# Kernel tuning notes

Measured on AMD Instinct MI355X. Metric: run time of the kernel, lower is better.

Reference implementation:

```python
import jax, jax.numpy as jnp
import numpy as np

N = 10000
IN_DIM = 256
HID = 256
HEADS = 8
NUM_CLASSES = 40
EPS = 1e-5
NEG_SLOPE = 0.2


def gat_conv(x, src, dst, W, a_src, a_dst, bias, concat):
    # x: [N, F_in]; W: [F_in, H*C]; a_src/a_dst: [H, C]
    n = x.shape[0]
    H, C = a_src.shape
    h = (x @ W).reshape(n, H, C)                       # [N,H,C]
    s_src = jnp.einsum('nhc,hc->nh', h, a_src)         # [N,H]
    s_dst = jnp.einsum('nhc,hc->nh', h, a_dst)         # [N,H]
    score = jax.nn.leaky_relu(s_src[src] + s_dst[dst], NEG_SLOPE)  # [E,H]
    m = jax.lax.stop_gradient(jax.ops.segment_max(score, dst, num_segments=n))
    e = jnp.exp(score - m[dst])                        # [E,H]
    denom = jax.ops.segment_sum(e, dst, num_segments=n)
    alpha = e / denom[dst]                             # per-dst edge softmax
    msg = h[src] * alpha[:, :, None]                   # [E,H,C]
    out = jax.ops.segment_sum(msg, dst, num_segments=n)  # [N,H,C]
    out = out.reshape(n, H * C) if concat else out.mean(axis=1)
    return out + bias


def batch_norm(x, gamma, beta):
    mu = x.mean(axis=0)
    var = x.var(axis=0)
    return gamma * (x - mu) * jax.lax.rsqrt(var + EPS) + beta


def setup_inputs() -> dict:
    key = jax.random.key(0)
    ks = jax.random.split(key, 16)
    C0 = HID // HEADS  # 32, concat layer
    x = jax.random.normal(ks[0], (N, IN_DIM), jnp.float32)
    edge_index = jax.random.randint(ks[1], (2, 160000), 0, N, jnp.int32)
    def lin(k, fi, fo):
        return jax.random.normal(k, (fi, fo), jnp.float32) / np.sqrt(fi)
    return {
        'x': x,
        'edge_index': edge_index,
        'W0': lin(ks[2], IN_DIM, HEADS * C0),
        'a_src0': jax.random.normal(ks[3], (HEADS, C0), jnp.float32) * 0.1,
        'a_dst0': jax.random.normal(ks[4], (HEADS, C0), jnp.float32) * 0.1,
        'b0': jnp.zeros((HID,), jnp.float32),
        'g0': jnp.ones((HID,), jnp.float32),
        'be0': jnp.zeros((HID,), jnp.float32),
        'W1': lin(ks[5], HID, HEADS * HID),
        'a_src1': jax.random.normal(ks[6], (HEADS, HID), jnp.float32) * 0.1,
        'a_dst1': jax.random.normal(ks[7], (HEADS, HID), jnp.float32) * 0.1,
        'b1': jnp.zeros((HID,), jnp.float32),
        'g1': jnp.ones((HID,), jnp.float32),
        'be1': jnp.zeros((HID,), jnp.float32),
        'Wc': lin(ks[8], HID, NUM_CLASSES),
        'bc': jnp.zeros((NUM_CLASSES,), jnp.float32),
    }


def reference(x, edge_index, W0, a_src0, a_dst0, b0, g0, be0,
              W1, a_src1, a_dst1, b1, g1, be1, Wc, bc):
    n = x.shape[0]
    loops = jnp.arange(n, dtype=edge_index.dtype)
    src = jnp.concatenate([edge_index[0], loops])  # add_self_loops=True
    dst = jnp.concatenate([edge_index[1], loops])

    # layer 0: concat=True -> [N, 256]
    h = gat_conv(x, src, dst, W0, a_src0, a_dst0, b0, concat=True)
    h = jax.nn.elu(batch_norm(h, g0, be0))
    # i==0: no residual; dropout is identity at eval

    # layer 1 (last): concat=False (mean over heads) -> [N, 256]
    h_in = h
    h = gat_conv(h, src, dst, W1, a_src1, a_dst1, b1, concat=False)
    h = jax.nn.elu(batch_norm(h, g1, be1)) + h_in  # residual for i>0

    return h @ Wc + bc  # logits [N, num_classes]
```

## Files before the change

### kernel.cpp

```cpp
#include <hip/hip_runtime.h>
#include <math.h>

#define NN 10000
#define HEADS 8
#define NCLS 40
#define CHK 64
#define LOG2E 1.4426950408889634f

typedef __attribute__((ext_vector_type(8))) short short8;
typedef __attribute__((ext_vector_type(4))) float floatx4;

static __device__ __forceinline__ short f2bf(float f) {
    unsigned u = __builtin_bit_cast(unsigned, f);
    unsigned r = (u + 0x7fff + ((u >> 16) & 1)) >> 16;
    return (short)r;
}
static __device__ __forceinline__ float bf2f(unsigned short u) {
    unsigned x = ((unsigned)u) << 16;
    return __builtin_bit_cast(float, x);
}
static __device__ __forceinline__ void gl2lds16(const void* g, void* l) {
    __builtin_amdgcn_global_load_lds(
        (const __attribute__((address_space(1))) unsigned int*)g,
        (__attribute__((address_space(3))) unsigned int*)l, 16, 0, 0);
}

__global__ __launch_bounds__(256) void gemm_bf16_v3(
    const short* __restrict__ A, const short* __restrict__ Bt,
    float* __restrict__ C, short* __restrict__ Cbf, const float* __restrict__ bias,
    float* __restrict__ stats, int M, int Nn, int K, float alpha)
{
    __shared__ short As[64 * 64];
    __shared__ short Bs[64 * 64];
    const int tid = threadIdx.x;
    const int w = tid >> 6, L = tid & 63;
    const int quad = L >> 4, lr = L & 15;
    const int col0 = blockIdx.x * 64, row0 = blockIdx.y * 64;

    const int srow = w * 16 + (L >> 3);
    const int schunk = (L & 7) ^ (L >> 3);
    int ga0 = row0 + srow;     if (ga0 > M - 1)  ga0 = M - 1;
    int ga1 = row0 + srow + 8; if (ga1 > M - 1)  ga1 = M - 1;
    int gb0 = col0 + srow;     if (gb0 > Nn - 1) gb0 = Nn - 1;
    int gb1 = col0 + srow + 8; if (gb1 > Nn - 1) gb1 = Nn - 1;
    const short* agp0 = A + (size_t)ga0 * K + schunk * 8;
    const short* agp1 = A + (size_t)ga1 * K + schunk * 8;
    const short* bgp0 = Bt + (size_t)gb0 * K + schunk * 8;
    const short* bgp1 = Bt + (size_t)gb1 * K + schunk * 8;
    short* alp0 = &As[w * 1024];
    short* alp1 = &As[w * 1024 + 512];
    short* blp0 = &Bs[w * 1024];
    short* blp1 = &Bs[w * 1024 + 512];

    floatx4 acc[4];
    const floatx4 zf = {0.f, 0.f, 0.f, 0.f};
    #pragma unroll
    for (int i = 0; i < 4; i++) acc[i] = zf;

    for (int k0 = 0; k0 < K; k0 += 64) {
        gl2lds16(agp0 + k0, alp0);
        gl2lds16(agp1 + k0, alp1);
        gl2lds16(bgp0 + k0, blp0);
        gl2lds16(bgp1 + k0, blp1);
        __syncthreads();
        #pragma unroll
        for (int ks = 0; ks < 2; ks++) {
            const int sl = ((ks * 4 + quad) ^ (lr & 7)) * 8;
            short8 bfr = *(const short8*)&Bs[(w * 16 + lr) * 64 + sl];
            #pragma unroll
            for (int i = 0; i < 4; i++) {
                short8 afr = *(const short8*)&As[(i * 16 + lr) * 64 + sl];
                acc[i] = __builtin_amdgcn_mfma_f32_16x16x32_bf16(afr, bfr, acc[i], 0, 0, 0);
            }
        }
        __syncthreads();
    }
    const int ccol = col0 + w * 16 + lr;
    float s = 0.f, s2 = 0.f;
    if (ccol < Nn) {
        float bv = bias ? bias[ccol] : 0.f;
        #pragma unroll
        for (int i = 0; i < 4; i++) {
            #pragma unroll
            for (int r = 0; r < 4; r++) {
                int crow = row0 + i * 16 + quad * 4 + r;
                if (crow < M) {
                    float v = alpha * acc[i][r] + bv;
                    if (C)   C[(size_t)crow * Nn + ccol] = v;
                    if (Cbf) Cbf[(size_t)crow * Nn + ccol] = f2bf(v);
                    s += v; s2 += v * v;
                }
            }
        }
    }
    if (stats) {
        s  += __shfl_xor(s, 16, 64);  s  += __shfl_xor(s, 32, 64);
        s2 += __shfl_xor(s2, 16, 64); s2 += __shfl_xor(s2, 32, 64);
        if (L < 16 && ccol < Nn) {
            atomicAdd(&stats[ccol], s);
            atomicAdd(&stats[256 + ccol], s2);
        }
    }
}

__global__ void count_edges_kernel(const int* __restrict__ dst, int* counts, int E) {
    int e = blockIdx.x * 256 + threadIdx.x;
    if (e < E) atomicAdd(&counts[dst[e]], 1);
}

__global__ __launch_bounds__(1024) void scan_kernel(
    int* counts, int* offsets, int* cursor, int* elist, int n)
{
    const int P = (n + 1023) >> 10;
    __shared__ int wsum[16];
    int tid = threadIdx.x, lane = tid & 63, wid = tid >> 6;
    int base = tid * P;
    int local[16];
    int deg[16];
    int s = 0;
    for (int j = 0; j < P; j++) {
        int i = base + j;
        local[j] = s;
        deg[j] = (i < n) ? counts[i] + 1 : 0;
        s += deg[j];
    }
    int inc = s;
    #pragma unroll
    for (int off = 1; off < 64; off <<= 1) {
        int tv = __shfl_up(inc, off, 64);
        if (lane >= off) inc += tv;
    }
    if (lane == 63) wsum[wid] = inc;
    __syncthreads();
    if (tid < 16) {
        int v = wsum[tid];
        int winc = v;
        #pragma unroll
        for (int off = 1; off < 16; off <<= 1) {
            int tv = __shfl_up(winc, off, 16);
            if (tid >= off) winc += tv;
        }
        wsum[tid] = winc - v;
    }
    __syncthreads();
    int excl = inc - s + wsum[wid];
    for (int j = 0; j < P; j++) {
        int i = base + j;
        if (i < n) {
            int o = excl + local[j];
            counts[i] = deg[j];
            offsets[i] = o;
            elist[o] = i;
            cursor[i] = o + 1;
        }
    }
}

__global__ void scatter_edges_kernel(const int* __restrict__ src, const int* __restrict__ dst,
                                     int* cursor, int* elist, int E) {
    int e = blockIdx.x * 256 + threadIdx.x;
    if (e < E) {
        int d = dst[e];
        int pos = atomicAdd(&cursor[d], 1);
        elist[pos] = src[e];
    }
}

__global__ __launch_bounds__(256) void prep_all(
    const float* __restrict__ x, const float* __restrict__ W0,
    const float* __restrict__ W1, const float* __restrict__ a_src1,
    const float* __restrict__ a_dst1, const float* __restrict__ Wc,
    short* __restrict__ xb, short* __restrict__ W0T, float* __restrict__ v1,
    short* __restrict__ W1pT, short* __restrict__ WcT)
{
    __shared__ float tile[32][33];
    const int b = blockIdx.x, t = threadIdx.x;
    if (b < 2500) {
        int i = b * 256 + t;
        floatx4 v = ((const floatx4*)x)[i];
        short4 o = {f2bf(v[0]), f2bf(v[1]), f2bf(v[2]), f2bf(v[3])};
        ((short4*)xb)[i] = o;
    } else if (b < 2756) {
        int o = b - 2500;
        W0T[o * 256 + t] = f2bf(W0[t * 256 + o]);
    } else if (b < 2772) {
        int idx = (b - 2756) * 256 + t;
        int f = idx >> 4, j = idx & 15;
        int h = j & 7;
        const float* a = (j < 8) ? a_src1 : a_dst1;
        float s = 0.f;
        for (int c = 0; c < 256; c++)
            s += W1[f * 2048 + h * 256 + c] * a[h * 256 + c];
        v1[idx] = s;
    } else if (b < 3284) {
        int id = b - 2772;
        int h = id >> 6, f0 = ((id >> 3) & 7) * 32, c0 = (id & 7) * 32;
        int tx = t & 31, ty = t >> 5;
        for (int r = ty; r < 32; r += 8)
            tile[r][tx] = W1[(size_t)(f0 + r) * 2048 + h * 256 + c0 + tx];
        __syncthreads();
        for (int r = ty; r < 32; r += 8)
            W1pT[(size_t)(c0 + r) * 2048 + h * 256 + f0 + tx] = f2bf(tile[tx][r]);
    } else {
        int o = b - 3284;
        WcT[o * 256 + t] = f2bf(Wc[t * 40 + o]);
    }
}

__global__ __launch_bounds__(256) void score0_wave(
    const unsigned short* __restrict__ h0b, const float* __restrict__ a_src,
    const float* __restrict__ a_dst, float* __restrict__ s0)
{
    const int wid = threadIdx.x >> 6, L = threadIdx.x & 63;
    const int n = blockIdx.x * 4 + wid;
    if (n >= NN) return;
    ushort4 vv = *(const ushort4*)(h0b + (size_t)n * 256 + 4 * L);
    floatx4 as = *(const floatx4*)(a_src + 4 * L);
    floatx4 ad = *(const floatx4*)(a_dst + 4 * L);
    float v0 = bf2f(vv.x), v1_ = bf2f(vv.y), v2 = bf2f(vv.z), v3 = bf2f(vv.w);
    float ps = v0 * as[0] + v1_ * as[1] + v2 * as[2] + v3 * as[3];
    float pd = v0 * ad[0] + v1_ * ad[1] + v2 * ad[2] + v3 * ad[3];
    #pragma unroll
    for (int off = 1; off < 8; off <<= 1) {
        ps += __shfl_xor(ps, off, 64);
        pd += __shfl_xor(pd, off, 64);
    }
    if ((L & 7) == 0) {
        s0[n * 16 + (L >> 3)] = ps;
        s0[n * 16 + 8 + (L >> 3)] = pd;
    }
}

__global__ __launch_bounds__(256) void agg0_fused(
    const unsigned short* __restrict__ h0b, const float* __restrict__ s0,
    const int* __restrict__ offsets, const int* __restrict__ counts,
    const int* __restrict__ elist, float* __restrict__ out)
{
    __shared__ float pw_s[4][CHK * 8];
    __shared__ int   sn_s[4][CHK];
    const int wid = threadIdx.x >> 6, L = threadIdx.x & 63;
    const int n = blockIdx.x * 4 + wid;
    if (n >= NN) return;
    float* pw = pw_s[wid];
    int*   sw = sn_s[wid];
    const int deg = counts[n], start = offsets[n];
    const int hL = L >> 3;

    floatx4 sda = *(const floatx4*)(s0 + n * 16 + 8);
    floatx4 sdb = *(const floatx4*)(s0 + n * 16 + 12);
    float sd[8] = {sda[0], sda[1], sda[2], sda[3], sdb[0], sdb[1], sdb[2], sdb[3]};
    float lp[8] = {0.f, 0.f, 0.f, 0.f, 0.f, 0.f, 0.f, 0.f};
    float a0 = 0.f, a1 = 0.f, a2 = 0.f, a3 = 0.f;

    for (int e0 = 0; e0 < deg; e0 += CHK) {
        int ch = deg - e0; if (ch > CHK) ch = CHK;
        if (L < ch) {
            int sn = elist[start + e0 + L];
            sw[L] = sn;
            floatx4 ssa = *(const floatx4*)(s0 + sn * 16);
            floatx4 ssb = *(const floatx4*)(s0 + sn * 16 + 4);
            float ss[8] = {ssa[0], ssa[1], ssa[2], ssa[3], ssb[0], ssb[1], ssb[2], ssb[3]};
            float p[8];
            #pragma unroll
            for (int h = 0; h < 8; h++) {
                float v = ss[h] + sd[h];
                v = (v > 0.f) ? v : 0.2f * v;
                p[h] = exp2f(v * LOG2E);
                lp[h] += p[h];
            }
            floatx4 p0 = {p[0], p[1], p[2], p[3]};
            floatx4 p1 = {p[4], p[5], p[6], p[7]};
            *(floatx4*)&pw[L * 8] = p0;
            *(floatx4*)&pw[L * 8 + 4] = p1;
        }
        for (int e = 0; e < ch; e++) {
            float wgt = pw[e * 8 + hL];
            ushort4 vv = *(const ushort4*)(h0b + (size_t)sw[e] * 256 + 4 * L);
            a0 += wgt * bf2f(vv.x);
            a1 += wgt * bf2f(vv.y);
            a2 += wgt * bf2f(vv.z);
            a3 += wgt * bf2f(vv.w);
        }
    }
    #pragma unroll
    for (int off = 1; off < 64; off <<= 1)
        #pragma unroll
        for (int h = 0; h < 8; h++)
            lp[h] += __shfl_xor(lp[h], off, 64);
    float inv = 1.f / lp[hL];
    floatx4 o = {a0 * inv, a1 * inv, a2 * inv, a3 * inv};
    *(floatx4*)(out + (size_t)n * 256 + 4 * L) = o;
}

__global__ __launch_bounds__(256) void agg1_fused(
    const unsigned short* __restrict__ hb, const float* __restrict__ s1,
    const int* __restrict__ offsets, const int* __restrict__ counts,
    const int* __restrict__ elist, short* __restrict__ aggout)
{
    __shared__ float pw_s[4][CHK * 8];
    __shared__ int   sn_s[4][CHK];
    const int wid = threadIdx.x >> 6, L = threadIdx.x & 63;
    const int n = blockIdx.x * 4 + wid;
    if (n >= NN) return;
    float* pw = pw_s[wid];
    int*   sw = sn_s[wid];
    const int deg = counts[n], start = offsets[n];

    floatx4 sda = *(const floatx4*)(s1 + n * 16 + 8);
    floatx4 sdb = *(const floatx4*)(s1 + n * 16 + 12);
    float sd[8] = {sda[0], sda[1], sda[2], sda[3], sdb[0], sdb[1], sdb[2], sdb[3]};
    float lp[8] = {0.f, 0.f, 0.f, 0.f, 0.f, 0.f, 0.f, 0.f};
    float acc[8][4];
    #pragma unroll
    for (int h = 0; h < 8; h++)
        #pragma unroll
        for (int f = 0; f < 4; f++) acc[h][f] = 0.f;

    for (int e0 = 0; e0 < deg; e0 += CHK) {
        int ch = deg - e0; if (ch > CHK) ch = CHK;
        if (L < ch) {
            int sn = elist[start + e0 + L];
            sw[L] = sn;
            floatx4 ssa = *(const floatx4*)(s1 + sn * 16);
            floatx4 ssb = *(const floatx4*)(s1 + sn * 16 + 4);
            float ss[8] = {ssa[0], ssa[1], ssa[2], ssa[3], ssb[0], ssb[1], ssb[2], ssb[3]};
            float p[8];
            #pragma unroll
            for (int h = 0; h < 8; h++) {
                float v = ss[h] + sd[h];
                v = (v > 0.f) ? v : 0.2f * v;
                p[h] = exp2f(v * LOG2E);
                lp[h] += p[h];
            }
            floatx4 p0 = {p[0], p[1], p[2], p[3]};
            floatx4 p1 = {p[4], p[5], p[6], p[7]};
            *(floatx4*)&pw[L * 8] = p0;
            *(floatx4*)&pw[L * 8 + 4] = p1;
        }
        for (int e = 0; e < ch; e++) {
            floatx4 pv0 = *(const floatx4*)&pw[e * 8];
            floatx4 pv1 = *(const floatx4*)&pw[e * 8 + 4];
            ushort4 vv = *(const ushort4*)(hb + (size_t)sw[e] * 256 + 4 * L);
            float v0 = bf2f(vv.x), v1_ = bf2f(vv.y), v2 = bf2f(vv.z), v3 = bf2f(vv.w);
            #pragma unroll
            for (int h = 0; h < 4; h++) {
                acc[h][0] += pv0[h] * v0;
                acc[h][1] += pv0[h] * v1_;
                acc[h][2] += pv0[h] * v2;
                acc[h][3] += pv0[h] * v3;
                acc[h + 4][0] += pv1[h] * v0;
                acc[h + 4][1] += pv1[h] * v1_;
                acc[h + 4][2] += pv1[h] * v2;
                acc[h + 4][3] += pv1[h] * v3;
            }
        }
    }
    #pragma unroll
    for (int off = 1; off < 64; off <<= 1)
        #pragma unroll
        for (int h = 0; h < 8; h++)
            lp[h] += __shfl_xor(lp[h], off, 64);
    #pragma unroll
    for (int h = 0; h < 8; h++) {
        float inv = 1.f / lp[h];
        short4 o = {f2bf(acc[h][0] * inv), f2bf(acc[h][1] * inv),
                    f2bf(acc[h][2] * inv), f2bf(acc[h][3] * inv)};
        *(short4*)(aggout + (size_t)n * 2048 + h * 256 + 4 * L) = o;
    }
}

__global__ __launch_bounds__(256) void bn_stats_kernel(const float* __restrict__ x, float* stats, int n) {
    int t = threadIdx.x;
    float s = 0.f, s2 = 0.f;
    for (int r = blockIdx.x; r < n; r += gridDim.x) {
        float v = x[(size_t)r * 256 + t];
        s += v; s2 += v * v;
    }
    atomicAdd(&stats[t], s);
    atomicAdd(&stats[256 + t], s2);
}

__global__ __launch_bounds__(256) void bnapply_score1(
    const float* __restrict__ xg, const float* __restrict__ stats,
    const float* __restrict__ g, const float* __restrict__ be,
    const float* __restrict__ v1, float* __restrict__ hact,
    short* __restrict__ hactb, float* __restrict__ s1)
{
    __shared__ float row[256];
    __shared__ float part[16][17];
    const int n = blockIdx.x, t = threadIdx.x;
    const float invN = 1.0f / NN;
    float mu = stats[t] * invN;
    float var = stats[256 + t] * invN - mu * mu;
    float v = g[t] * (xg[(size_t)n * 256 + t] - mu) * rsqrtf(var + 1e-5f) + be[t];
    v = (v > 0.f) ? v : (expf(v) - 1.f);
    hact[(size_t)n * 256 + t] = v;
    hactb[(size_t)n * 256 + t] = f2bf(v);
    row[t] = v;
    __syncthreads();
    int j = t & 15, f0 = t >> 4;
    float p = 0.f;
    #pragma unroll
    for (int k = 0; k < 16; k++)
        p += row[f0 * 16 + k] * v1[(f0 * 16 + k) * 16 + j];
    part[f0][j] = p;
    __syncthreads();
    if (t < 16) {
        float s = 0.f;
        #pragma unroll
        for (int k = 0; k < 16; k++) s += part[k][t];
        s1[n * 16 + t] = s;
    }
}

__global__ __launch_bounds__(256) void bn_apply_kernel(
    const float* __restrict__ x, const float* __restrict__ stats,
    const float* __restrict__ g, const float* __restrict__ be,
    const float* __restrict__ resid, short* __restrict__ ybf, int total)
{
    int i = blockIdx.x * 256 + threadIdx.x;
    if (i >= total) return;
    int c = i & 255;
    const float invN = 1.0f / NN;
    float mu = stats[c] * invN;
    float var = stats[256 + c] * invN - mu * mu;
    float v = g[c] * (x[i] - mu) * rsqrtf(var + 1e-5f) + be[c];
    v = (v > 0.f) ? v : (expf(v) - 1.f);
    v += resid[i];
    ybf[i] = f2bf(v);
}

extern "C" void kernel_launch(void* const* d_in, const int* in_sizes, int n_in,
                              void* d_out, int out_size, void* d_ws, size_t ws_size,
                              hipStream_t stream) {
    const float* x      = (const float*)d_in[0];
    const int*   eidx   = (const int*)d_in[1];
    const float* W0     = (const float*)d_in[2];
    const float* a_src0 = (const float*)d_in[3];
    const float* a_dst0 = (const float*)d_in[4];
    const float* g0     = (const float*)d_in[6];
    const float* be0    = (const float*)d_in[7];
    const float* W1     = (const float*)d_in[8];
    const float* a_src1 = (const float*)d_in[9];
    const float* a_dst1 = (const float*)d_in[10];
    const float* g1     = (const float*)d_in[12];
    const float* be1    = (const float*)d_in[13];
    const float* Wc     = (const float*)d_in[14];
    const float* bc     = (const float*)d_in[15];
    float* out = (float*)d_out;

    const int E = in_sizes[1] / 2;
    const int* esrc = eidx;
    const int* edst = eidx + E;

    char* ws = (char*)d_ws;
    size_t off = 0;
    auto alloc = [&](size_t bytes) {
        void* p = ws + off;
        off += (bytes + 255) & ~(size_t)255;
        return p;
    };
    float* stats   = (float*)alloc(1024 * 4);
    int*   counts  = (int*)alloc(NN * 4);
    float* out1    = (float*)alloc((size_t)NN * 256 * 4);
    short* h0b     = (short*)alloc((size_t)NN * 256 * 2);
    short* xb      = (short*)alloc((size_t)NN * 256 * 2);
    float* s0      = (float*)alloc((size_t)NN * 16 * 4);
    float* s1      = (float*)alloc((size_t)NN * 16 * 4);
    float* v1      = (float*)alloc(4096 * 4);
    float* h_gat0  = (float*)alloc((size_t)NN * 256 * 4);
    float* hact    = (float*)alloc((size_t)NN * 256 * 4);
    short* hactb   = (short*)alloc((size_t)NN * 256 * 2);
    short* agg1bf  = (short*)alloc((size_t)NN * 2048 * 2);
    short* W0T     = (short*)alloc((size_t)256 * 256 * 2);
    short* W1pT    = (short*)alloc((size_t)256 * 2048 * 2);
    short* WcT     = (short*)alloc((size_t)64 * 256 * 2);
    short* hfinbf  = (short*)alloc((size_t)NN * 256 * 2);
    int* offsets   = (int*)alloc((NN + 16) * 4);
    int* cursor    = (int*)alloc(NN * 4);
    int* elist     = (int*)alloc((size_t)(E + NN) * 4);

    float* stats0 = stats;
    float* stats1 = stats + 512;

    hipMemsetAsync(stats, 0, 1024 * 4 + NN * 4, stream);

    count_edges_kernel<<<(E + 255) / 256, 256, 0, stream>>>(edst, counts, E);
    scan_kernel<<<1, 1024, 0, stream>>>(counts, offsets, cursor, elist, NN);
    scatter_edges_kernel<<<(E + 255) / 256, 256, 0, stream>>>(esrc, edst, cursor, elist, E);

    prep_all<<<3324, 256, 0, stream>>>(x, W0, W1, a_src1, a_dst1, Wc,
                                       xb, W0T, v1, W1pT, WcT);

    {
        dim3 grid(4, (NN + 63) / 64);
        gemm_bf16_v3<<<grid, 256, 0, stream>>>(xb, W0T, nullptr, h0b, nullptr, nullptr,
                                               NN, 256, 256, 1.0f);
    }
    score0_wave<<<(NN + 3) / 4, 256, 0, stream>>>(
        (const unsigned short*)h0b, a_src0, a_dst0, s0);
    agg0_fused<<<(NN + 3) / 4, 256, 0, stream>>>(
        (const unsigned short*)h0b, s0, offsets, counts, elist, h_gat0);
    bn_stats_kernel<<<256, 256, 0, stream>>>(h_gat0, stats0, NN);
    bnapply_score1<<<NN, 256, 0, stream>>>(h_gat0, stats0, g0, be0, v1, hact, hactb, s1);

    agg1_fused<<<(NN + 3) / 4, 256, 0, stream>>>(
        (const unsigned short*)hactb, s1, offsets, counts, elist, agg1bf);
    {
        dim3 grid(4, (NN + 63) / 64);
        gemm_bf16_v3<<<grid, 256, 0, stream>>>(agg1bf, W1pT, out1, nullptr, nullptr, stats1,
                                               NN, 256, 2048, 0.125f);
    }
    bn_apply_kernel<<<(NN * 256 + 255) / 256, 256, 0, stream>>>(
        out1, stats1, g1, be1, hact, hfinbf, NN * 256);

    {
        dim3 grid(1, (NN + 63) / 64);
        gemm_bf16_v3<<<grid, 256, 0, stream>>>(hfinbf, WcT, out, nullptr, bc, nullptr,
                                               NN, NCLS, 256, 1.0f);
    }
}
```

Baseline: 273.2 us.

## Fuse BN stats into agg0, fuse final BN+residual with classifier, drop fp32 copy

The layer-0 batch-norm statistics are now accumulated inside the aggregation kernel through a block-level shared-memory reduction and atomics, which removes the separate stats pass over the 10 MB activation. The final batch-norm apply, residual add and 40-class classifier are merged into one per-row kernel, replacing an elementwise kernel plus a bf16 GEMM and the Wc transpose. The fp32 copy of the hidden activation is dropped, so the residual is read back from its bf16 copy, which costs some precision. Bounds checks are removed because NN divides evenly by 4, and the scalar per-row classifier dot product may be slower than the MFMA GEMM it replaces.

```diff
diff --git a/kernel.cpp b/kernel.cpp
--- a/kernel.cpp
+++ b/kernel.cpp
@@ -169,9 +169,9 @@
 __global__ __launch_bounds__(256) void prep_all(
     const float* __restrict__ x, const float* __restrict__ W0,
     const float* __restrict__ W1, const float* __restrict__ a_src1,
-    const float* __restrict__ a_dst1, const float* __restrict__ Wc,
+    const float* __restrict__ a_dst1,
     short* __restrict__ xb, short* __restrict__ W0T, float* __restrict__ v1,
-    short* __restrict__ W1pT, short* __restrict__ WcT)
+    short* __restrict__ W1pT)
 {
     __shared__ float tile[32][33];
     const int b = blockIdx.x, t = threadIdx.x;
@@ -192,7 +192,7 @@
         for (int c = 0; c < 256; c++)
             s += W1[f * 2048 + h * 256 + c] * a[h * 256 + c];
         v1[idx] = s;
-    } else if (b < 3284) {
+    } else {
         int id = b - 2772;
         int h = id >> 6, f0 = ((id >> 3) & 7) * 32, c0 = (id & 7) * 32;
         int tx = t & 31, ty = t >> 5;
@@ -201,9 +201,6 @@
         __syncthreads();
         for (int r = ty; r < 32; r += 8)
             W1pT[(size_t)(c0 + r) * 2048 + h * 256 + f0 + tx] = f2bf(tile[tx][r]);
-    } else {
-        int o = b - 3284;
-        WcT[o * 256 + t] = f2bf(Wc[t * 40 + o]);
     }
 }
 
@@ -213,7 +210,6 @@
 {
     const int wid = threadIdx.x >> 6, L = threadIdx.x & 63;
     const int n = blockIdx.x * 4 + wid;
-    if (n >= NN) return;
     ushort4 vv = *(const ushort4*)(h0b + (size_t)n * 256 + 4 * L);
     floatx4 as = *(const floatx4*)(a_src + 4 * L);
     floatx4 ad = *(const floatx4*)(a_dst + 4 * L);
@@ -234,13 +230,13 @@
 __global__ __launch_bounds__(256) void agg0_fused(
     const unsigned short* __restrict__ h0b, const float* __restrict__ s0,
     const int* __restrict__ offsets, const int* __restrict__ counts,
-    const int* __restrict__ elist, float* __restrict__ out)
+    const int* __restrict__ elist, float* __restrict__ out,
+    float* __restrict__ stats)
 {
     __shared__ float pw_s[4][CHK * 8];
     __shared__ int   sn_s[4][CHK];
     const int wid = threadIdx.x >> 6, L = threadIdx.x & 63;
     const int n = blockIdx.x * 4 + wid;
-    if (n >= NN) return;
     float* pw = pw_s[wid];
     int*   sw = sn_s[wid];
     const int deg = counts[n], start = offsets[n];
@@ -290,6 +286,16 @@
     float inv = 1.f / lp[hL];
     floatx4 o = {a0 * inv, a1 * inv, a2 * inv, a3 * inv};
     *(floatx4*)(out + (size_t)n * 256 + 4 * L) = o;
+
+    floatx4 o2 = {o[0] * o[0], o[1] * o[1], o[2] * o[2], o[3] * o[3]};
+    *(floatx4*)&pw[4 * L] = o;
+    *(floatx4*)&pw[256 + 4 * L] = o2;
+    __syncthreads();
+    int c = threadIdx.x;
+    float sc_ = pw_s[0][c] + pw_s[1][c] + pw_s[2][c] + pw_s[3][c];
+    float sc2 = pw_s[0][256 + c] + pw_s[1][256 + c] + pw_s[2][256 + c] + pw_s[3][256 + c];
+    atomicAdd(&stats[c], sc_);
+    atomicAdd(&stats[256 + c], sc2);
 }
 
 __global__ __launch_bounds__(256) void agg1_fused(
@@ -301,7 +307,6 @@
     __shared__ int   sn_s[4][CHK];
     const int wid = threadIdx.x >> 6, L = threadIdx.x & 63;
     const int n = blockIdx.x * 4 + wid;
-    if (n >= NN) return;
     float* pw = pw_s[wid];
     int*   sw = sn_s[wid];
     const int deg = counts[n], start = offsets[n];
@@ -369,22 +374,10 @@
     }
 }
 
-__global__ __launch_bounds__(256) void bn_stats_kernel(const float* __restrict__ x, float* stats, int n) {
-    int t = threadIdx.x;
-    float s = 0.f, s2 = 0.f;
-    for (int r = blockIdx.x; r < n; r += gridDim.x) {
-        float v = x[(size_t)r * 256 + t];
-        s += v; s2 += v * v;
-    }
-    atomicAdd(&stats[t], s);
-    atomicAdd(&stats[256 + t], s2);
-}
-
 __global__ __launch_bounds__(256) void bnapply_score1(
     const float* __restrict__ xg, const float* __restrict__ stats,
     const float* __restrict__ g, const float* __restrict__ be,
-    const float* __restrict__ v1, float* __restrict__ hact,
-    short* __restrict__ hactb, float* __restrict__ s1)
+    const float* __restrict__ v1, short* __restrict__ hactb, float* __restrict__ s1)
 {
     __shared__ float row[256];
     __shared__ float part[16][17];
@@ -394,7 +387,6 @@
     float var = stats[256 + t] * invN - mu * mu;
     float v = g[t] * (xg[(size_t)n * 256 + t] - mu) * rsqrtf(var + 1e-5f) + be[t];
     v = (v > 0.f) ? v : (expf(v) - 1.f);
-    hact[(size_t)n * 256 + t] = v;
     hactb[(size_t)n * 256 + t] = f2bf(v);
     row[t] = v;
     __syncthreads();
@@ -413,21 +405,46 @@
     }
 }
 
-__global__ __launch_bounds__(256) void bn_apply_kernel(
-    const float* __restrict__ x, const float* __restrict__ stats,
+__global__ __launch_bounds__(256) void bnapply_cls(
+    const float* __restrict__ out1, const float* __restrict__ stats,
     const float* __restrict__ g, const float* __restrict__ be,
-    const float* __restrict__ resid, short* __restrict__ ybf, int total)
-{
-    int i = blockIdx.x * 256 + threadIdx.x;
-    if (i >= total) return;
-    int c = i & 255;
+    const unsigned short* __restrict__ hactb, const float* __restrict__ Wc,
+    const float* __restrict__ bc, float* __restrict__ out)
+{
+    __shared__ float row[256];
+    __shared__ float part[16][17];
+    const int n = blockIdx.x, t = threadIdx.x;
     const float invN = 1.0f / NN;
-    float mu = stats[c] * invN;
-    float var = stats[256 + c] * invN - mu * mu;
-    float v = g[c] * (x[i] - mu) * rsqrtf(var + 1e-5f) + be[c];
+    float mu = stats[t] * invN;
+    float var = stats[256 + t] * invN - mu * mu;
+    float v = g[t] * (out1[(size_t)n * 256 + t] - mu) * rsqrtf(var + 1e-5f) + be[t];
     v = (v > 0.f) ? v : (expf(v) - 1.f);
-    v += resid[i];
-    ybf[i] = f2bf(v);
+    v += bf2f(hactb[(size_t)n * 256 + t]);
+    row[t] = v;
+    __syncthreads();
+    const int j16 = t & 15, f0 = t >> 4;
+    #pragma unroll
+    for (int grp = 0; grp < 3; grp++) {
+        int col = grp * 16 + j16;
+        float p = 0.f;
+        if (col < NCLS) {
+            #pragma unroll
+            for (int k = 0; k < 16; k++)
+                p += row[f0 * 16 + k] * Wc[(f0 * 16 + k) * NCLS + col];
+        }
+        part[f0][j16] = p;
+        __syncthreads();
+        if (t < 16) {
+            int c = grp * 16 + t;
+            if (c < NCLS) {
+                float s = 0.f;
+                #pragma unroll
+                for (int k = 0; k < 16; k++) s += part[k][t];
+                out[(size_t)n * NCLS + c] = s + bc[c];
+            }
+        }
+        __syncthreads();
+    }
 }
 
 extern "C" void kernel_launch(void* const* d_in, const int* in_sizes, int n_in,
@@ -469,13 +486,10 @@
     float* s1      = (float*)alloc((size_t)NN * 16 * 4);
     float* v1      = (float*)alloc(4096 * 4);
     float* h_gat0  = (float*)alloc((size_t)NN * 256 * 4);
-    float* hact    = (float*)alloc((size_t)NN * 256 * 4);
     short* hactb   = (short*)alloc((size_t)NN * 256 * 2);
     short* agg1bf  = (short*)alloc((size_t)NN * 2048 * 2);
     short* W0T     = (short*)alloc((size_t)256 * 256 * 2);
     short* W1pT    = (short*)alloc((size_t)256 * 2048 * 2);
-    short* WcT     = (short*)alloc((size_t)64 * 256 * 2);
-    short* hfinbf  = (short*)alloc((size_t)NN * 256 * 2);
     int* offsets   = (int*)alloc((NN + 16) * 4);
     int* cursor    = (int*)alloc(NN * 4);
     int* elist     = (int*)alloc((size_t)(E + NN) * 4);
@@ -489,34 +503,28 @@
     scan_kernel<<<1, 1024, 0, stream>>>(counts, offsets, cursor, elist, NN);
     scatter_edges_kernel<<<(E + 255) / 256, 256, 0, stream>>>(esrc, edst, cursor, elist, E);
 
-    prep_all<<<3324, 256, 0, stream>>>(x, W0, W1, a_src1, a_dst1, Wc,
-                                       xb, W0T, v1, W1pT, WcT);
+    prep_all<<<3284, 256, 0, stream>>>(x, W0, W1, a_src1, a_dst1,
+                                       xb, W0T, v1, W1pT);
 
     {
         dim3 grid(4, (NN + 63) / 64);
         gemm_bf16_v3<<<grid, 256, 0, stream>>>(xb, W0T, nullptr, h0b, nullptr, nullptr,
                                                NN, 256, 256, 1.0f);
     }
-    score0_wave<<<(NN + 3) / 4, 256, 0, stream>>>(
+    score0_wave<<<NN / 4, 256, 0, stream>>>(
         (const unsigned short*)h0b, a_src0, a_dst0, s0);
-    agg0_fused<<<(NN + 3) / 4, 256, 0, stream>>>(
-        (const unsigned short*)h0b, s0, offsets, counts, elist, h_gat0);
-    bn_stats_kernel<<<256, 256, 0, stream>>>(h_gat0, stats0, NN);
-    bnapply_score1<<<NN, 256, 0, stream>>>(h_gat0, stats0, g0, be0, v1, hact, hactb, s1);
-
-    agg1_fused<<<(NN + 3) / 4, 256, 0, stream>>>(
+    agg0_fused<<<NN / 4, 256, 0, stream>>>(
+        (const unsigned short*)h0b, s0, offsets, counts, elist, h_gat0, stats0);
+    bnapply_score1<<<NN, 256, 0, stream>>>(h_gat0, stats0, g0, be0, v1, hactb, s1);
+
+    agg1_fused<<<NN / 4, 256, 0, stream>>>(
         (const unsigned short*)hactb, s1, offsets, counts, elist, agg1bf);
     {
         dim3 grid(4, (NN + 63) / 64);
         gemm_bf16_v3<<<grid, 256, 0, stream>>>(agg1bf, W1pT, out1, nullptr, nullptr, stats1,
                                                NN, 256, 2048, 0.125f);
     }
-    bn_apply_kernel<<<(NN * 256 + 255) / 256, 256, 0, stream>>>(
-        out1, stats1, g1, be1, hact, hfinbf, NN * 256);
-
-    {
-        dim3 grid(1, (NN + 63) / 64);
-        gemm_bf16_v3<<<grid, 256, 0, stream>>>(hfinbf, WcT, out, nullptr, bc, nullptr,
-                                               NN, NCLS, 256, 1.0f);
-    }
-}
+
+    bnapply_cls<<<NN, 256, 0, stream>>>(out1, stats1, g1, be1,
+                                        (const unsigned short*)hactb, Wc, bc, out);
+}
```

Result: slower. 327.6 us (+19.9%).

## Split layer-1 aggregation across head halves, fuse edge counting into prep, drop fp32 residual

Applied to the files above, without the earlier changes.

The layer-1 aggregation kernel now gives each node two waves, each handling four of the eight heads. This halves per-wave accumulator registers and doubles the wave count, which should improve occupancy and latency hiding on the gather. Edge counting is merged into the weight-prep kernel to save a launch. The fp32 residual copy is dropped, and the residual is read back from the bf16 activation instead, cutting memory traffic at the cost of some residual precision. Bounds checks are also removed, which relies on N being divisible by 4.

```diff
diff --git a/kernel.cpp b/kernel.cpp
--- a/kernel.cpp
+++ b/kernel.cpp
@@ -103,11 +103,6 @@
     }
 }
 
-__global__ void count_edges_kernel(const int* __restrict__ dst, int* counts, int E) {
-    int e = blockIdx.x * 256 + threadIdx.x;
-    if (e < E) atomicAdd(&counts[dst[e]], 1);
-}
-
 __global__ __launch_bounds__(1024) void scan_kernel(
     int* counts, int* offsets, int* cursor, int* elist, int n)
 {
@@ -166,12 +161,13 @@
     }
 }
 
-__global__ __launch_bounds__(256) void prep_all(
+__global__ __launch_bounds__(256) void prep_count(
     const float* __restrict__ x, const float* __restrict__ W0,
     const float* __restrict__ W1, const float* __restrict__ a_src1,
     const float* __restrict__ a_dst1, const float* __restrict__ Wc,
+    const int* __restrict__ edst, int E,
     short* __restrict__ xb, short* __restrict__ W0T, float* __restrict__ v1,
-    short* __restrict__ W1pT, short* __restrict__ WcT)
+    short* __restrict__ W1pT, short* __restrict__ WcT, int* __restrict__ counts)
 {
     __shared__ float tile[32][33];
     const int b = blockIdx.x, t = threadIdx.x;
@@ -201,9 +197,12 @@
         __syncthreads();
         for (int r = ty; r < 32; r += 8)
             W1pT[(size_t)(c0 + r) * 2048 + h * 256 + f0 + tx] = f2bf(tile[tx][r]);
-    } else {
+    } else if (b < 3324) {
         int o = b - 3284;
         WcT[o * 256 + t] = f2bf(Wc[t * 40 + o]);
+    } else {
+        int e = (b - 3324) * 256 + t;
+        if (e < E) atomicAdd(&counts[edst[e]], 1);
     }
 }
 
@@ -213,7 +212,6 @@
 {
     const int wid = threadIdx.x >> 6, L = threadIdx.x & 63;
     const int n = blockIdx.x * 4 + wid;
-    if (n >= NN) return;
     ushort4 vv = *(const ushort4*)(h0b + (size_t)n * 256 + 4 * L);
     floatx4 as = *(const floatx4*)(a_src + 4 * L);
     floatx4 ad = *(const floatx4*)(a_dst + 4 * L);
@@ -240,7 +238,6 @@
     __shared__ int   sn_s[4][CHK];
     const int wid = threadIdx.x >> 6, L = threadIdx.x & 63;
     const int n = blockIdx.x * 4 + wid;
-    if (n >= NN) return;
     float* pw = pw_s[wid];
     int*   sw = sn_s[wid];
     const int deg = counts[n], start = offsets[n];
@@ -292,27 +289,25 @@
     *(floatx4*)(out + (size_t)n * 256 + 4 * L) = o;
 }
 
-__global__ __launch_bounds__(256) void agg1_fused(
+__global__ __launch_bounds__(256) void agg1_half(
     const unsigned short* __restrict__ hb, const float* __restrict__ s1,
     const int* __restrict__ offsets, const int* __restrict__ counts,
     const int* __restrict__ elist, short* __restrict__ aggout)
 {
-    __shared__ float pw_s[4][CHK * 8];
+    __shared__ float pw_s[4][CHK * 4];
     __shared__ int   sn_s[4][CHK];
     const int wid = threadIdx.x >> 6, L = threadIdx.x & 63;
-    const int n = blockIdx.x * 4 + wid;
-    if (n >= NN) return;
+    const int n = blockIdx.x * 2 + (wid >> 1);
+    const int hg = wid & 1;
     float* pw = pw_s[wid];
     int*   sw = sn_s[wid];
     const int deg = counts[n], start = offsets[n];
 
-    floatx4 sda = *(const floatx4*)(s1 + n * 16 + 8);
-    floatx4 sdb = *(const floatx4*)(s1 + n * 16 + 12);
-    float sd[8] = {sda[0], sda[1], sda[2], sda[3], sdb[0], sdb[1], sdb[2], sdb[3]};
-    float lp[8] = {0.f, 0.f, 0.f, 0.f, 0.f, 0.f, 0.f, 0.f};
-    float acc[8][4];
-    #pragma unroll
-    for (int h = 0; h < 8; h++)
+    floatx4 sd4 = *(const floatx4*)(s1 + n * 16 + 8 + hg * 4);
+    float lp[4] = {0.f, 0.f, 0.f, 0.f};
+    float acc[4][4];
+    #pragma unroll
+    for (int h = 0; h < 4; h++)
         #pragma unroll
         for (int f = 0; f < 4; f++) acc[h][f] = 0.f;
 
@@ -321,51 +316,42 @@
         if (L < ch) {
             int sn = elist[start + e0 + L];
             sw[L] = sn;
-            floatx4 ssa = *(const floatx4*)(s1 + sn * 16);
-            floatx4 ssb = *(const floatx4*)(s1 + sn * 16 + 4);
-            float ss[8] = {ssa[0], ssa[1], ssa[2], ssa[3], ssb[0], ssb[1], ssb[2], ssb[3]};
-            float p[8];
+            floatx4 ss4 = *(const floatx4*)(s1 + sn * 16 + hg * 4);
+            floatx4 p4;
             #pragma unroll
-            for (int h = 0; h < 8; h++) {
-                float v = ss[h] + sd[h];
+            for (int h = 0; h < 4; h++) {
+                float v = ss4[h] + sd4[h];
                 v = (v > 0.f) ? v : 0.2f * v;
-                p[h] = exp2f(v * LOG2E);
-                lp[h] += p[h];
+                float p = exp2f(v * LOG2E);
+                p4[h] = p;
+                lp[h] += p;
             }
-            floatx4 p0 = {p[0], p[1], p[2], p[3]};
-            floatx4 p1 = {p[4], p[5], p[6], p[7]};
-            *(floatx4*)&pw[L * 8] = p0;
-            *(floatx4*)&pw[L * 8 + 4] = p1;
+            *(floatx4*)&pw[L * 4] = p4;
         }
         for (int e = 0; e < ch; e++) {
-            floatx4 pv0 = *(const floatx4*)&pw[e * 8];
-            floatx4 pv1 = *(const floatx4*)&pw[e * 8 + 4];
+            floatx4 pv = *(const floatx4*)&pw[e * 4];
             ushort4 vv = *(const ushort4*)(hb + (size_t)sw[e] * 256 + 4 * L);
             float v0 = bf2f(vv.x), v1_ = bf2f(vv.y), v2 = bf2f(vv.z), v3 = bf2f(vv.w);
             #pragma unroll
             for (int h = 0; h < 4; h++) {
-                acc[h][0] += pv0[h] * v0;
-                acc[h][1] += pv0[h] * v1_;
-                acc[h][2] += pv0[h] * v2;
-                acc[h][3] += pv0[h] * v3;
-                acc[h + 4][0] += pv1[h] * v0;
-                acc[h + 4][1] += pv1[h] * v1_;
-                acc[h + 4][2] += pv1[h] * v2;
-                acc[h + 4][3] += pv1[h] * v3;
+                acc[h][0] += pv[h] * v0;
+                acc[h][1] += pv[h] * v1_;
+                acc[h][2] += pv[h] * v2;
+                acc[h][3] += pv[h] * v3;
             }
         }
     }
     #pragma unroll
     for (int off = 1; off < 64; off <<= 1)
         #pragma unroll
-        for (int h = 0; h < 8; h++)
+        for (int h = 0; h < 4; h++)
             lp[h] += __shfl_xor(lp[h], off, 64);
     #pragma unroll
-    for (int h = 0; h < 8; h++) {
+    for (int h = 0; h < 4; h++) {
         float inv = 1.f / lp[h];
         short4 o = {f2bf(acc[h][0] * inv), f2bf(acc[h][1] * inv),
                     f2bf(acc[h][2] * inv), f2bf(acc[h][3] * inv)};
-        *(short4*)(aggout + (size_t)n * 2048 + h * 256 + 4 * L) = o;
+        *(short4*)(aggout + (size_t)n * 2048 + (hg * 4 + h) * 256 + 4 * L) = o;
     }
 }
 
@@ -383,8 +369,7 @@
 __global__ __launch_bounds__(256) void bnapply_score1(
     const float* __restrict__ xg, const float* __restrict__ stats,
     const float* __restrict__ g, const float* __restrict__ be,
-    const float* __restrict__ v1, float* __restrict__ hact,
-    short* __restrict__ hactb, float* __restrict__ s1)
+    const float* __restrict__ v1, short* __restrict__ hactb, float* __restrict__ s1)
 {
     __shared__ float row[256];
     __shared__ float part[16][17];
@@ -394,7 +379,6 @@
     float var = stats[256 + t] * invN - mu * mu;
     float v = g[t] * (xg[(size_t)n * 256 + t] - mu) * rsqrtf(var + 1e-5f) + be[t];
     v = (v > 0.f) ? v : (expf(v) - 1.f);
-    hact[(size_t)n * 256 + t] = v;
     hactb[(size_t)n * 256 + t] = f2bf(v);
     row[t] = v;
     __syncthreads();
@@ -416,7 +400,7 @@
 __global__ __launch_bounds__(256) void bn_apply_kernel(
     const float* __restrict__ x, const float* __restrict__ stats,
     const float* __restrict__ g, const float* __restrict__ be,
-    const float* __restrict__ resid, short* __restrict__ ybf, int total)
+    const unsigned short* __restrict__ resid, short* __restrict__ ybf, int total)
 {
     int i = blockIdx.x * 256 + threadIdx.x;
     if (i >= total) return;
@@ -426,7 +410,7 @@
     float var = stats[256 + c] * invN - mu * mu;
     float v = g[c] * (x[i] - mu) * rsqrtf(var + 1e-5f) + be[c];
     v = (v > 0.f) ? v : (expf(v) - 1.f);
-    v += resid[i];
+    v += bf2f(resid[i]);
     ybf[i] = f2bf(v);
 }
 
@@ -469,7 +453,6 @@
     float* s1      = (float*)alloc((size_t)NN * 16 * 4);
     float* v1      = (float*)alloc(4096 * 4);
     float* h_gat0  = (float*)alloc((size_t)NN * 256 * 4);
-    float* hact    = (float*)alloc((size_t)NN * 256 * 4);
     short* hactb   = (short*)alloc((size_t)NN * 256 * 2);
     short* agg1bf  = (short*)alloc((size_t)NN * 2048 * 2);
     short* W0T     = (short*)alloc((size_t)256 * 256 * 2);
@@ -485,26 +468,27 @@
 
     hipMemsetAsync(stats, 0, 1024 * 4 + NN * 4, stream);
 
-    count_edges_kernel<<<(E + 255) / 256, 256, 0, stream>>>(edst, counts, E);
+    const int cntBlocks = (E + 255) / 256;
+    prep_count<<<3324 + cntBlocks, 256, 0, stream>>>(
+        x, W0, W1, a_src1, a_dst1, Wc, edst, E,
+        xb, W0T, v1, W1pT, WcT, counts);
+
     scan_kernel<<<1, 1024, 0, stream>>>(counts, offsets, cursor, elist, NN);
-    scatter_edges_kernel<<<(E + 255) / 256, 256, 0, stream>>>(esrc, edst, cursor, elist, E);
-
-    prep_all<<<3324, 256, 0, stream>>>(x, W0, W1, a_src1, a_dst1, Wc,
-                                       xb, W0T, v1, W1pT, WcT);
+    scatter_edges_kernel<<<cntBlocks, 256, 0, stream>>>(esrc, edst, cursor, elist, E);
 
     {
         dim3 grid(4, (NN + 63) / 64);
         gemm_bf16_v3<<<grid, 256, 0, stream>>>(xb, W0T, nullptr, h0b, nullptr, nullptr,
                                                NN, 256, 256, 1.0f);
     }
-    score0_wave<<<(NN + 3) / 4, 256, 0, stream>>>(
+    score0_wave<<<NN / 4, 256, 0, stream>>>(
         (const unsigned short*)h0b, a_src0, a_dst0, s0);
-    agg0_fused<<<(NN + 3) / 4, 256, 0, stream>>>(
+    agg0_fused<<<NN / 4, 256, 0, stream>>>(
         (const unsigned short*)h0b, s0, offsets, counts, elist, h_gat0);
     bn_stats_kernel<<<256, 256, 0, stream>>>(h_gat0, stats0, NN);
-    bnapply_score1<<<NN, 256, 0, stream>>>(h_gat0, stats0, g0, be0, v1, hact, hactb, s1);
-
-    agg1_fused<<<(NN + 3) / 4, 256, 0, stream>>>(
+    bnapply_score1<<<NN, 256, 0, stream>>>(h_gat0, stats0, g0, be0, v1, hactb, s1);
+
+    agg1_half<<<NN / 2, 256, 0, stream>>>(
         (const unsigned short*)hactb, s1, offsets, counts, elist, agg1bf);
     {
         dim3 grid(4, (NN + 63) / 64);
@@ -512,7 +496,7 @@
                                                NN, 256, 2048, 0.125f);
     }
     bn_apply_kernel<<<(NN * 256 + 255) / 256, 256, 0, stream>>>(
-        out1, stats1, g1, be1, hact, hfinbf, NN * 256);
+        out1, stats1, g1, be1, (const unsigned short*)hactb, hfinbf, NN * 256);
 
     {
         dim3 grid(1, (NN + 63) / 64);
```

After: 272.4 us. No clear change (-0.3%).
